# Kernel optimization log

Hardware: AMD Instinct MI355X
Metric: run time of the kernel (lower is better)

## Reference

```python
import jax, jax.numpy as jnp
import numpy as np

BEV_H = 200
BEV_W = 200
H_METERS = 100.0
W_METERS = 100.0
THRESHOLD = 0.05
LOW_PASS = 0.3  # 3DGS screen-space low-pass filter added to cov2D diagonal
ALPHA_MIN = 1.0 / 255.0
ALPHA_MAX = 0.99


def setup_inputs() -> dict:
    key = jax.random.key(0)
    k1, k2, k3, k4 = jax.random.split(key, 4)
    B, G, D = 2, 2000, 32
    features = jax.random.normal(k1, (B, G, D), dtype=jnp.float32)
    # means uniformly covering the [-50, 50] x [-50, 50] BEV extent (z unused)
    means3D = (jax.random.uniform(k2, (B, G, 3), dtype=jnp.float32) - 0.5) * 100.0
    # PSD 3x3 covariances, ~1-2 m std -> a few pixels at 2 px/m
    A = jax.random.normal(k3, (B, G, 3, 3), dtype=jnp.float32)
    Sigma = jnp.einsum('bgij,bgkj->bgik', A, A) + 0.1 * jnp.eye(3, dtype=jnp.float32)
    iu = jnp.triu_indices(3)
    cov3D = Sigma[:, :, iu[0], iu[1]]  # b g 6 : (xx, xy, xz, yy, yz, zz)
    opacities = jax.random.uniform(k4, (B, G, 1), dtype=jnp.float32)
    return {'features': features, 'means3D': means3D, 'cov3D': cov3D,
            'opacities': opacities}


def _render(features, means3D, cov3D, opacities):
    B, G, D = features.shape
    sh = BEV_H / H_METERS  # 2 px / m
    sw = BEV_W / W_METERS
    op = opacities[..., 0]                      # b g
    mask = op > THRESHOLD                       # opacity gating (torch masks rows;
                                                # zero-alpha is mathematically identical)
    # orthographic BEV projection (full_proj_transform rows 0 and 1)
    x, y = means3D[..., 0], means3D[..., 1]
    u = -sh * y + BEV_H / 2.0                   # row coordinate, b g
    v = -sw * x + BEV_W / 2.0                   # col coordinate, b g
    # cov2D = M Sigma M^T with M = [[0, sh, 0], [sw, 0, 0]], plus low-pass
    sxx, sxy, syy = cov3D[..., 0], cov3D[..., 1], cov3D[..., 3]
    c00 = sh * sh * syy + LOW_PASS
    c01 = sh * sw * sxy
    c11 = sw * sw * sxx + LOW_PASS
    det = c00 * c11 - c01 * c01
    valid = mask & (det > 0.0)
    inv_det = jnp.where(det > 0.0, 1.0 / jnp.where(det > 0.0, det, 1.0), 0.0)
    cA = c11 * inv_det                          # conic (A, B, C)
    cB = -c01 * inv_det
    cC = c00 * inv_det
    # per-pixel Gaussian power, separably broadcast: [b g H 1] + [b g 1 W]
    gi = jnp.arange(BEV_H, dtype=jnp.float32)
    gj = jnp.arange(BEV_W, dtype=jnp.float32)
    du = u[..., None] - gi                      # b g H
    dv = v[..., None] - gj                      # b g W
    power = (-0.5 * cA)[..., None, None] * (du * du)[..., :, None] \
          + (-0.5 * cC)[..., None, None] * (dv * dv)[..., None, :] \
          + (-cB)[..., None, None] * du[..., :, None] * dv[..., None, :]  # b g H W
    alpha = jnp.minimum(ALPHA_MAX, op[..., None, None] * jnp.exp(power))
    keep = valid[..., None, None] & (power <= 0.0) & (alpha >= ALPHA_MIN)
    alpha = jnp.where(keep, alpha, 0.0)
    alpha = alpha.reshape(B, G, BEV_H * BEV_W)  # b g p
    # front-to-back alpha compositing: exclusive cumprod of transmittance
    T_excl = jnp.concatenate(
        [jnp.ones((B, 1, BEV_H * BEV_W), dtype=alpha.dtype),
         jnp.cumprod(1.0 - alpha, axis=1)[:, :-1]], axis=1)
    weight = alpha * T_excl                     # b g p
    out = jnp.einsum('bgp,bgd->bdp', weight, features)  # bg_color is zeros
    out = out.reshape(B, D, BEV_H, BEV_W)
    num_gaussians = jnp.mean(jnp.sum(mask.astype(jnp.float32), axis=1))
    return out, num_gaussians


def reference(features, means3D, cov3D, opacities):
    return _render(features, means3D, cov3D, opacities)
```

## Files before the change

### kernel.cpp

```cpp
#include <hip/hip_runtime.h>
#include <math.h>

#define BEV_H 200
#define BEV_W 200
#define NPIX (BEV_H * BEV_W)
#define TILE 8
#define NT 25
#define NB 2
#define T_DEAD 1e-10f
#define SEGCAP 512
#define KC 32
#define NLOG255 (-5.5412635f)

__global__ __launch_bounds__(256) void precompute_kernel(
    const float* __restrict__ means3D, const float* __restrict__ cov3D,
    const float* __restrict__ opac, float4* __restrict__ params,
    float4* __restrict__ bbox, int n )
{
    const int idx = blockIdx.x * 256 + threadIdx.x;
    if (idx >= n) return;
    const float x = means3D[idx * 3 + 0], y = means3D[idx * 3 + 1];
    const float sxx = cov3D[idx * 6 + 0], sxy = cov3D[idx * 6 + 1],
                syy = cov3D[idx * 6 + 3];
    const float op = opac[idx];
    const float u = -2.0f * y + 100.0f;
    const float v = -2.0f * x + 100.0f;
    const float c00 = 4.0f * syy + 0.3f;
    const float c01 = 4.0f * sxy;
    const float c11 = 4.0f * sxx + 0.3f;
    const float det = c00 * c11 - c01 * c01;
    float4 bb = make_float4(1e9f, -1e9f, 1e9f, -1e9f);
    float qa = 0.f, qb = 0.f, qc = 0.f, lop = 0.f;
    if (op > 0.05f && det > 0.0f) {
        const float inv = 1.0f / det;
        qa = -0.5f * (c11 * inv);
        qb = c01 * inv;
        qc = -0.5f * (c00 * inv);
        lop = logf(op);
        const float L = logf(255.0f * op);
        const float ru = sqrtf(2.0f * L * c00) + 0.01f;
        const float rv = sqrtf(2.0f * L * c11) + 0.01f;
        bb = make_float4(u - ru, u + ru, v - rv, v + rv);
    }
    params[idx * 2 + 0] = make_float4(u, v, qa, qb);
    params[idx * 2 + 1] = make_float4(qc, lop, 0.0f, 0.0f);
    bbox[idx] = bb;
}

__device__ __forceinline__ unsigned pk2bf(float x, float y)
{
    unsigned ux = __float_as_uint(x), uy = __float_as_uint(y);
    ux = ux + 0x7fffu + ((ux >> 16) & 1u);
    uy = uy + 0x7fffu + ((uy >> 16) & 1u);
    return (ux >> 16) | (uy & 0xffff0000u);
}

__global__ __launch_bounds__(256) void render_tile_kernel(
    const float* __restrict__ features, const float4* __restrict__ params,
    const float4* __restrict__ bbox, float* __restrict__ out, int G)
{
    __shared__ int   slist[4][SEGCAP];
    __shared__ float4 plA[4][KC];
    __shared__ float2 plB[4][KC];
    __shared__ uint4  flq[4][KC][4];
    __shared__ float  xch[2][64][33];

    const int tid  = threadIdx.x;
    const int lane = tid & 63;
    const int w    = tid >> 6;
    const int b  = blockIdx.z;
    const int tj = blockIdx.x;
    const int ti = blockIdx.y;
    const int j = tj * TILE + (lane & 7);
    const int i = ti * TILE + (lane >> 3);
    const float fi = (float)i, fj = (float)j;
    const float ti_lo = (float)(ti * TILE), ti_hi = ti_lo + (TILE - 1);
    const float tj_lo = (float)(tj * TILE), tj_hi = tj_lo + (TILE - 1);
    const int gbase = b * G;

    const int g_lo = (w * G) >> 2;
    const int g_hi = ((w + 1) * G) >> 2;

    int tot = 0;
    for (int g0 = g_lo; g0 < g_hi; g0 += 64) {
        const int g = g0 + lane;
        bool keep = false;
        if (g < g_hi) {
            const float4 bb = bbox[gbase + g];
            keep = (bb.y >= ti_lo) && (bb.x <= ti_hi) &&
                   (bb.w >= tj_lo) && (bb.z <= tj_hi);
        }
        const unsigned long long bal = __ballot(keep);
        if (keep) {
            const int pre = (int)__popcll(bal & ((1ull << lane) - 1ull));
            slist[w][tot + pre] = g;
        }
        tot += (int)__popcll(bal);
    }

    float acc[32];
#pragma unroll
    for (int d = 0; d < 32; ++d) acc[d] = 0.0f;
    float T = 1.0f;

    for (int k0 = 0; k0 < tot; k0 += KC) {
        if (!__any(T >= T_DEAD)) break;
        const int nk = min(KC, tot - k0);

        if (lane < nk) {
            const int g = slist[w][k0 + lane];
            const float4* pp = params + (size_t)(gbase + g) * 2;
            const float4 a = pp[0];
            const float4 c = pp[1];
            plA[w][lane] = a;
            plB[w][lane] = make_float2(c.x, c.y);
        }
        for (int idx = lane; idx < nk * 4; idx += 64) {
            const int e = idx >> 2, q = idx & 3;
            const int g = slist[w][k0 + e];
            const float4* fp =
                (const float4*)(features + (size_t)(gbase + g) * 32) + q * 2;
            const float4 A = fp[0], B = fp[1];
            flq[w][e][q] = make_uint4(pk2bf(A.x, A.y), pk2bf(A.z, A.w),
                                      pk2bf(B.x, B.y), pk2bf(B.z, B.w));
        }

#pragma unroll 2
        for (int k = 0; k < nk; ++k) {
            const float4 pA = plA[w][k];
            const float2 pB = plB[w][k];
            const float du = pA.x - fi;
            const float dv = pA.y - fj;
            const float power = pA.z * du * du + pB.x * dv * dv + pA.w * du * dv;
            const float powb = power + pB.y;
            float alpha = fminf(0.99f, __expf(powb));
            const bool ok = (powb >= NLOG255) && (power <= 0.0f);
            alpha = ok ? alpha : 0.0f;
            const float wgt = alpha * T;
            T *= 1.0f - alpha;
#pragma unroll
            for (int q = 0; q < 4; ++q) {
                const uint4 uq = flq[w][k][q];
                const unsigned uu[4] = {uq.x, uq.y, uq.z, uq.w};
#pragma unroll
                for (int c = 0; c < 4; ++c) {
                    const float lo = __uint_as_float(uu[c] << 16);
                    const float hi = __uint_as_float(uu[c] & 0xffff0000u);
                    acc[q * 8 + c * 2 + 0] = fmaf(wgt, lo, acc[q * 8 + c * 2 + 0]);
                    acc[q * 8 + c * 2 + 1] = fmaf(wgt, hi, acc[q * 8 + c * 2 + 1]);
                }
            }
        }
    }

    if (w == 1 || w == 3) {
        float* row = xch[(w - 1) >> 1][lane];
#pragma unroll
        for (int d = 0; d < 32; ++d) row[d] = acc[d];
        row[32] = T;
    }
    __syncthreads();
    if (w == 0 || w == 2) {
        const float* row = xch[w >> 1][lane];
        const float Tn = row[32];
#pragma unroll
        for (int d = 0; d < 32; ++d) acc[d] = fmaf(T, row[d], acc[d]);
        T *= Tn;
    }
    __syncthreads();
    if (w == 2) {
        float* row = xch[0][lane];
#pragma unroll
        for (int d = 0; d < 32; ++d) row[d] = acc[d];
        row[32] = T;
    }
    __syncthreads();
    if (w == 0) {
        const float* row = xch[0][lane];
#pragma unroll
        for (int d = 0; d < 32; ++d) acc[d] = fmaf(T, row[d], acc[d]);

        const int p = i * BEV_W + j;
        float* ob = out + (size_t)b * 32 * NPIX + p;
#pragma unroll
        for (int d = 0; d < 32; ++d) ob[(size_t)d * NPIX] = acc[d];
    }
}

__global__ __launch_bounds__(256) void count_kernel(
    const float* __restrict__ opac, float* __restrict__ out, int n, int out_idx)
{
    __shared__ float sdata[256];
    const int tid = threadIdx.x;
    float s = 0.0f;
    for (int idx = tid; idx < n; idx += 256)
        s += (opac[idx] > 0.05f) ? 1.0f : 0.0f;
    sdata[tid] = s;
    __syncthreads();
    for (int off = 128; off > 0; off >>= 1) {
        if (tid < off) sdata[tid] += sdata[tid + off];
        __syncthreads();
    }
    if (tid == 0) out[out_idx] = sdata[0] * (1.0f / NB);
}

extern "C" void kernel_launch(void* const* d_in, const int* in_sizes, int n_in,
                              void* d_out, int out_size, void* d_ws, size_t ws_size,
                              hipStream_t stream)
{
    const float* features = (const float*)d_in[0];
    const float* means3D  = (const float*)d_in[1];
    const float* cov3D    = (const float*)d_in[2];
    const float* opac     = (const float*)d_in[3];
    float* out = (float*)d_out;

    const int G = in_sizes[3] / NB;
    const int n = NB * G;

    float4* params = (float4*)d_ws;
    float4* bbox   = params + (size_t)n * 2;

    precompute_kernel<<<(n + 255) / 256, 256, 0, stream>>>(
        means3D, cov3D, opac, params, bbox, n);

    dim3 grid(NT, NT, NB);
    render_tile_kernel<<<grid, 256, 0, stream>>>(features, params, bbox, out, G);

    count_kernel<<<1, 256, 0, stream>>>(opac, out, n, NB * 32 * NPIX);
}
```

Measured before the change: 92.01 us.

## Fuse preprocessing and count into tile render kernel, recompute params per tile

Removes the separate precompute and count kernels. Each tile block now reads raw means, covariances and opacities, computes bounding radii on the fly with software prefetch of the next round, and recomputes conic parameters for the Gaussians it keeps. The opacity count is done by one wave of block (0,0,0). This saves two launches and the params/bbox round trip through memory. In exchange every one of 1250 blocks repeats the per-Gaussian log/sqrt work and makes strided raw loads, which may cost more than the launches it saves.

```diff
diff --git a/kernel.cpp b/kernel.cpp
--- a/kernel.cpp
+++ b/kernel.cpp
@@ -12,41 +12,6 @@
 #define KC 32
 #define NLOG255 (-5.5412635f)
 
-__global__ __launch_bounds__(256) void precompute_kernel(
-    const float* __restrict__ means3D, const float* __restrict__ cov3D,
-    const float* __restrict__ opac, float4* __restrict__ params,
-    float4* __restrict__ bbox, int n )
-{
-    const int idx = blockIdx.x * 256 + threadIdx.x;
-    if (idx >= n) return;
-    const float x = means3D[idx * 3 + 0], y = means3D[idx * 3 + 1];
-    const float sxx = cov3D[idx * 6 + 0], sxy = cov3D[idx * 6 + 1],
-                syy = cov3D[idx * 6 + 3];
-    const float op = opac[idx];
-    const float u = -2.0f * y + 100.0f;
-    const float v = -2.0f * x + 100.0f;
-    const float c00 = 4.0f * syy + 0.3f;
-    const float c01 = 4.0f * sxy;
-    const float c11 = 4.0f * sxx + 0.3f;
-    const float det = c00 * c11 - c01 * c01;
-    float4 bb = make_float4(1e9f, -1e9f, 1e9f, -1e9f);
-    float qa = 0.f, qb = 0.f, qc = 0.f, lop = 0.f;
-    if (op > 0.05f && det > 0.0f) {
-        const float inv = 1.0f / det;
-        qa = -0.5f * (c11 * inv);
-        qb = c01 * inv;
-        qc = -0.5f * (c00 * inv);
-        lop = logf(op);
-        const float L = logf(255.0f * op);
-        const float ru = sqrtf(2.0f * L * c00) + 0.01f;
-        const float rv = sqrtf(2.0f * L * c11) + 0.01f;
-        bb = make_float4(u - ru, u + ru, v - rv, v + rv);
-    }
-    params[idx * 2 + 0] = make_float4(u, v, qa, qb);
-    params[idx * 2 + 1] = make_float4(qc, lop, 0.0f, 0.0f);
-    bbox[idx] = bb;
-}
-
 __device__ __forceinline__ unsigned pk2bf(float x, float y)
 {
     unsigned ux = __float_as_uint(x), uy = __float_as_uint(y);
@@ -55,11 +20,12 @@
     return (ux >> 16) | (uy & 0xffff0000u);
 }
 
-__global__ __launch_bounds__(256) void render_tile_kernel(
-    const float* __restrict__ features, const float4* __restrict__ params,
-    const float4* __restrict__ bbox, float* __restrict__ out, int G)
+__global__ __launch_bounds__(256) void render_fused_kernel(
+    const float* __restrict__ features, const float* __restrict__ means3D,
+    const float* __restrict__ cov3D, const float* __restrict__ opac,
+    float* __restrict__ out, int G)
 {
-    __shared__ int   slist[4][SEGCAP];
+    __shared__ int    glist[4][SEGCAP];
     __shared__ float4 plA[4][KC];
     __shared__ float2 plB[4][KC];
     __shared__ uint4  flq[4][KC][4];
@@ -77,25 +43,49 @@
     const float ti_lo = (float)(ti * TILE), ti_hi = ti_lo + (TILE - 1);
     const float tj_lo = (float)(tj * TILE), tj_hi = tj_lo + (TILE - 1);
     const int gbase = b * G;
-
     const int g_lo = (w * G) >> 2;
     const int g_hi = ((w + 1) * G) >> 2;
+    const int rounds = (g_hi - g_lo + 63) >> 6;
 
     int tot = 0;
-    for (int g0 = g_lo; g0 < g_hi; g0 += 64) {
-        const int g = g0 + lane;
-        bool keep = false;
-        if (g < g_hi) {
-            const float4 bb = bbox[gbase + g];
-            keep = (bb.y >= ti_lo) && (bb.x <= ti_hi) &&
-                   (bb.w >= tj_lo) && (bb.z <= tj_hi);
-        }
-        const unsigned long long bal = __ballot(keep);
-        if (keep) {
-            const int pre = (int)__popcll(bal & ((1ull << lane) - 1ull));
-            slist[w][tot + pre] = g;
-        }
-        tot += (int)__popcll(bal);
+    {
+        int gg = min(g_lo + lane, g_hi - 1);
+        size_t gi = (size_t)(gbase + gg);
+        float x0 = means3D[gi * 3 + 0], y0 = means3D[gi * 3 + 1];
+        float s0 = cov3D[gi * 6 + 0], s1 = cov3D[gi * 6 + 1], s3 = cov3D[gi * 6 + 3];
+        float o0 = opac[gi];
+        for (int r = 0; r < rounds; ++r) {
+            float x1 = 0.f, y1 = 0.f, t0 = 0.f, t1 = 0.f, t3 = 0.f, o1 = 0.f;
+            if (r + 1 < rounds) {
+                const int gn = min(g_lo + (r + 1) * 64 + lane, g_hi - 1);
+                const size_t gni = (size_t)(gbase + gn);
+                x1 = means3D[gni * 3 + 0]; y1 = means3D[gni * 3 + 1];
+                t0 = cov3D[gni * 6 + 0];   t1 = cov3D[gni * 6 + 1];
+                t3 = cov3D[gni * 6 + 3];   o1 = opac[gni];
+            }
+            const int g = g_lo + r * 64 + lane;
+            const float u = -2.0f * y0 + 100.0f;
+            const float v = -2.0f * x0 + 100.0f;
+            const float c00 = 4.0f * s3 + 0.3f;
+            const float c01 = 4.0f * s1;
+            const float c11 = 4.0f * s0 + 0.3f;
+            const float det = c00 * c11 - c01 * c01;
+            bool keep = false;
+            if (o0 > 0.05f && det > 0.0f && g < g_hi) {
+                const float L = __logf(255.0f * o0);
+                const float ru = sqrtf(2.0f * L * c00) + 0.01f;
+                const float rv = sqrtf(2.0f * L * c11) + 0.01f;
+                keep = (u + ru >= ti_lo) && (u - ru <= ti_hi) &&
+                       (v + rv >= tj_lo) && (v - rv <= tj_hi);
+            }
+            const unsigned long long bal = __ballot(keep);
+            if (keep) {
+                const int pre = (int)__popcll(bal & ((1ull << lane) - 1ull));
+                glist[w][tot + pre] = g;
+            }
+            tot += (int)__popcll(bal);
+            x0 = x1; y0 = y1; s0 = t0; s1 = t1; s3 = t3; o0 = o1;
+        }
     }
 
     float acc[32];
@@ -108,21 +98,29 @@
         const int nk = min(KC, tot - k0);
 
         if (lane < nk) {
-            const int g = slist[w][k0 + lane];
-            const float4* pp = params + (size_t)(gbase + g) * 2;
-            const float4 a = pp[0];
-            const float4 c = pp[1];
-            plA[w][lane] = a;
-            plB[w][lane] = make_float2(c.x, c.y);
+            const int g = glist[w][k0 + lane];
+            const size_t gi = (size_t)(gbase + g);
+            const float x = means3D[gi * 3 + 0], y = means3D[gi * 3 + 1];
+            const float sxx = cov3D[gi * 6 + 0], sxy = cov3D[gi * 6 + 1],
+                        syy = cov3D[gi * 6 + 3];
+            const float op = opac[gi];
+            const float u = -2.0f * y + 100.0f;
+            const float v = -2.0f * x + 100.0f;
+            const float c00 = 4.0f * syy + 0.3f;
+            const float c01 = 4.0f * sxy;
+            const float c11 = 4.0f * sxx + 0.3f;
+            const float inv = 1.0f / (c00 * c11 - c01 * c01);
+            plA[w][lane] = make_float4(u, v, -0.5f * c11 * inv, c01 * inv);
+            plB[w][lane] = make_float2(-0.5f * c00 * inv, __logf(op));
         }
         for (int idx = lane; idx < nk * 4; idx += 64) {
             const int e = idx >> 2, q = idx & 3;
-            const int g = slist[w][k0 + e];
+            const int g = glist[w][k0 + e];
             const float4* fp =
                 (const float4*)(features + (size_t)(gbase + g) * 32) + q * 2;
-            const float4 A = fp[0], B = fp[1];
+            const float4 A = fp[0], Bq = fp[1];
             flq[w][e][q] = make_uint4(pk2bf(A.x, A.y), pk2bf(A.z, A.w),
-                                      pk2bf(B.x, B.y), pk2bf(B.z, B.w));
+                                      pk2bf(Bq.x, Bq.y), pk2bf(Bq.z, Bq.w));
         }
 
 #pragma unroll 2
@@ -175,6 +173,7 @@
         row[32] = T;
     }
     __syncthreads();
+
     if (w == 0) {
         const float* row = xch[0][lane];
 #pragma unroll
@@ -185,23 +184,20 @@
 #pragma unroll
         for (int d = 0; d < 32; ++d) ob[(size_t)d * NPIX] = acc[d];
     }
-}
-
-__global__ __launch_bounds__(256) void count_kernel(
-    const float* __restrict__ opac, float* __restrict__ out, int n, int out_idx)
-{
-    __shared__ float sdata[256];
-    const int tid = threadIdx.x;
-    float s = 0.0f;
-    for (int idx = tid; idx < n; idx += 256)
-        s += (opac[idx] > 0.05f) ? 1.0f : 0.0f;
-    sdata[tid] = s;
-    __syncthreads();
-    for (int off = 128; off > 0; off >>= 1) {
-        if (tid < off) sdata[tid] += sdata[tid + off];
-        __syncthreads();
-    }
-    if (tid == 0) out[out_idx] = sdata[0] * (1.0f / NB);
+
+    if (w == 1 && blockIdx.x == 0 && blockIdx.y == 0 && blockIdx.z == 0) {
+        const float4* o4 = (const float4*)opac;
+        const int n4 = (NB * G) >> 2;
+        float s = 0.0f;
+        for (int idx = lane; idx < n4; idx += 64) {
+            const float4 o = o4[idx];
+            s += (o.x > 0.05f ? 1.0f : 0.0f) + (o.y > 0.05f ? 1.0f : 0.0f) +
+                 (o.z > 0.05f ? 1.0f : 0.0f) + (o.w > 0.05f ? 1.0f : 0.0f);
+        }
+#pragma unroll
+        for (int off = 32; off > 0; off >>= 1) s += __shfl_down(s, off);
+        if (lane == 0) out[NB * 32 * NPIX] = s * (1.0f / NB);
+    }
 }
 
 extern "C" void kernel_launch(void* const* d_in, const int* in_sizes, int n_in,
@@ -215,16 +211,8 @@
     float* out = (float*)d_out;
 
     const int G = in_sizes[3] / NB;
-    const int n = NB * G;
-
-    float4* params = (float4*)d_ws;
-    float4* bbox   = params + (size_t)n * 2;
-
-    precompute_kernel<<<(n + 255) / 256, 256, 0, stream>>>(
-        means3D, cov3D, opac, params, bbox, n);
 
     dim3 grid(NT, NT, NB);
-    render_tile_kernel<<<grid, 256, 0, stream>>>(features, params, bbox, out, G);
-
-    count_kernel<<<1, 256, 0, stream>>>(opac, out, n, NB * 32 * NPIX);
+    render_fused_kernel<<<grid, 256, 0, stream>>>(features, means3D, cov3D, opac,
+                                                  out, G);
 }
```

After: 84.01 us. 8.7% less time.
